# Kernel optimization log

Measured on AMD Instinct MI355X. Metric: run time of the kernel, lower is better.

The kernel has to match this reference:

```python
import jax, jax.numpy as jnp
import numpy as np
from jax import lax

B, CIN, COUT, N, H, W = 8, 64, 64, 9, 128, 128
KS, PAD = 3, 1
EPS = 1e-5
DN = ('NCHW', 'OIHW', 'NCHW')

def _conv(x, w, b, pad):
    y = lax.conv_general_dilated(x, w, (1, 1), [(pad, pad), (pad, pad)], dimension_numbers=DN)
    return y + b[None, :, None, None]

def setup_inputs() -> dict:
    key = jax.random.key(0)
    ks = jax.random.split(key, 8)
    fan = CIN * KS * KS
    s = 1.0 / np.sqrt(fan)
    return {
        'x': jax.random.normal(ks[0], (B, CIN, H, W), dtype=jnp.float32),
        'kernels_w': jax.random.uniform(ks[1], (N, COUT, CIN, KS, KS), minval=-s, maxval=s, dtype=jnp.float32),
        'kernels_b': jax.random.uniform(ks[2], (N, COUT), minval=-s, maxval=s, dtype=jnp.float32),
        'obs1_w': jax.random.uniform(ks[3], (COUT // 2, CIN, 1, 1), minval=-1/np.sqrt(CIN), maxval=1/np.sqrt(CIN), dtype=jnp.float32),
        'obs1_b': jax.random.uniform(ks[4], (COUT // 2,), minval=-1/np.sqrt(CIN), maxval=1/np.sqrt(CIN), dtype=jnp.float32),
        'obs2_w': jax.random.uniform(ks[5], (N, COUT // 2, 1, 1), minval=-1/np.sqrt(COUT // 2), maxval=1/np.sqrt(COUT // 2), dtype=jnp.float32),
        'obs2_b': jax.random.uniform(ks[6], (N,), minval=-1/np.sqrt(COUT // 2), maxval=1/np.sqrt(COUT // 2), dtype=jnp.float32),
        'gamma': jnp.ones((COUT,), dtype=jnp.float32),
        'beta': jnp.zeros((COUT,), dtype=jnp.float32),
    }

def reference(x, kernels_w, kernels_b, obs1_w, obs1_b, obs2_w, obs2_b, gamma, beta):
    b, _, h, w = x.shape
    # all N path convs as one grouped-output conv: (B, N*COUT, H, W)
    paths = _conv(x, kernels_w.reshape(N * COUT, CIN, KS, KS), kernels_b.reshape(-1), PAD)
    paths = paths.reshape(b, N, COUT, h, w)
    # observer: 1x1 conv -> tanh -> 1x1 conv, scores (B, N, H, W)
    scores = _conv(jnp.tanh(_conv(x, obs1_w, obs1_b, 0)), obs2_w, obs2_b, 0)
    # eval-mode collapse: per-pixel argmax over paths, one-hot weighted sum == gather
    idx = jnp.argmax(scores, axis=1)  # (B, H, W)
    sel = jnp.take_along_axis(paths, idx[:, None, None, :, :], axis=1)[:, 0]  # (B, COUT, H, W)
    out = jax.nn.relu(sel)
    # ModularPhaseNorm2d (assumed instance-norm-style per-channel spatial norm with affine)
    mu = jnp.mean(out, axis=(2, 3), keepdims=True)
    var = jnp.var(out, axis=(2, 3), keepdims=True)
    y = (out - mu) * lax.rsqrt(var + EPS)
    return y * gamma[None, :, None, None] + beta[None, :, None, None]
```

## Files before the change

kernel.cpp:

```cpp
#include <hip/hip_runtime.h>
#include <hip/hip_bf16.h>
#include <stdint.h>

#define B_    8
#define CIN   64
#define COUT  64
#define NPATH 9
#define H_    128
#define W_    128
#define HW    16384
#define PTOT  131072
#define NBIN  72
#define CHUNK 64
#define NBLK  256
#define MAXCHUNK 4096
#define NSCORE 1024

typedef float  f32x4   __attribute__((ext_vector_type(4)));
typedef float  f32x16  __attribute__((ext_vector_type(16)));
typedef __bf16 bf16x8  __attribute__((ext_vector_type(8)));
typedef short  short8  __attribute__((ext_vector_type(8)));
typedef unsigned short ushort4v __attribute__((ext_vector_type(4)));

__device__ __forceinline__ short f2bf(float f) {
    __bf16 b = (__bf16)f;
    return __builtin_bit_cast(short, b);
}
__device__ __forceinline__ float bf2f(unsigned short u) {
    unsigned v = ((unsigned)u) << 16;
    return __builtin_bit_cast(float, v);
}
__device__ __forceinline__ float fast_tanh(float a) {
    float e = __builtin_amdgcn_exp2f(a * 2.885390081777927f);
    return 1.0f - 2.0f / (e + 1.0f);
}

#define GC(arr, i)  ((arr)[(i) * 16])
#define SM(arr, i)  ((arr)[(i) * 16])

__global__ void k_zero(f32x4* __restrict__ dst) {
    int i = blockIdx.x * 256 + threadIdx.x;
    if (i < 5120) dst[i] = (f32x4)0.0f;
}

__global__ __launch_bounds__(256, 2) void k_pre(
                      const float* __restrict__ x,
                      const float* __restrict__ w1, const float* __restrict__ b1,
                      const float* __restrict__ w2, const float* __restrict__ b2,
                      const float* __restrict__ kw,
                      unsigned* __restrict__ gcnt, unsigned* __restrict__ lists,
                      unsigned short* __restrict__ Xb,
                      unsigned short* __restrict__ WbF) {
    int t = threadIdx.x;
    if (blockIdx.x >= NSCORE) {
        int ob = ((int)blockIdx.x - NSCORE) * 4096 + t * 16;
        #pragma unroll
        for (int j = 0; j < 16; ++j) {
            int o = ob + j;
            int jj   = o & 7;
            int lane = (o >> 3) & 63;
            int f    = (o >> 9) & 3;
            int rest = o >> 11;
            int s    = rest % 18;
            int n    = rest / 18;
            int c    = f * 16 + (lane & 15);
            int kg   = lane >> 4;
            int ci   = ((s & 1) << 5) + (kg << 3) + jj;
            int tap  = s >> 1;
            WbF[o] = (unsigned short)f2bf(kw[((n * 64 + c) * 64 + ci) * 9 + tap]);
        }
        return;
    }
    __shared__ float xt[64 * 128];
    __shared__ float ht[32 * 128];
    __shared__ float w1t[64 * 36];
    __shared__ unsigned scnt[NBIN];
    __shared__ unsigned sbase[NBIN];

    int px0 = blockIdx.x * 128;
    int b   = blockIdx.x >> 7;
    int hw0 = px0 & 16383;
    if (t < NBIN) scnt[t] = 0u;

    const float* xbp = x + (((size_t)b) << 20) + hw0;
    #pragma unroll
    for (int i = 0; i < 8; ++i) {
        int flat = i * 256 + t;
        int ch = flat >> 5, ck = flat & 31;
        f32x4 v = *(const f32x4*)(xbp + ch * HW + ck * 4);
        *(f32x4*)(&xt[ch * 128 + ck * 4]) = v;
    }
    #pragma unroll
    for (int i = 0; i < 8; ++i) {
        int flat = i * 256 + t;
        int j = flat >> 6, ch = flat & 63;
        w1t[ch * 36 + j] = w1[flat];
    }
    __syncthreads();

    int wv = t >> 6, l = t & 63;
    {
        float acc[8][2];
        #pragma unroll
        for (int jj = 0; jj < 8; ++jj) {
            float bj = b1[wv * 8 + jj];
            acc[jj][0] = bj; acc[jj][1] = bj;
        }
        #pragma unroll 8
        for (int ch = 0; ch < 64; ++ch) {
            f32x4 wa = *(const f32x4*)(&w1t[ch * 36 + wv * 8]);
            f32x4 wb = *(const f32x4*)(&w1t[ch * 36 + wv * 8 + 4]);
            float2 xx = *(const float2*)(&xt[ch * 128 + l * 2]);
            #pragma unroll
            for (int jj = 0; jj < 4; ++jj) {
                acc[jj][0]     += xx.x * wa[jj];
                acc[jj][1]     += xx.y * wa[jj];
                acc[4 + jj][0] += xx.x * wb[jj];
                acc[4 + jj][1] += xx.y * wb[jj];
            }
        }
        #pragma unroll
        for (int jj = 0; jj < 8; ++jj)
            *(float2*)(&ht[(wv * 8 + jj) * 128 + l * 2]) =
                make_float2(acc[jj][0], acc[jj][1]);
    }
    __syncthreads();

    int bin = 0; unsigned rank = 0;
    if (t < 128) {
        int px = t;
        float h[32];
        #pragma unroll
        for (int j = 0; j < 32; ++j) h[j] = fast_tanh(ht[j * 128 + px]);
        float best = -1e30f; int bi = 0;
        #pragma unroll
        for (int nn = 0; nn < 9; ++nn) {
            const f32x16 Wa = *(const f32x16*)&w2[nn * 32];
            const f32x16 Wb = *(const f32x16*)&w2[nn * 32 + 16];
            float a = b2[nn];
            #pragma unroll
            for (int i = 0; i < 16; ++i)
                a += h[i] * Wa[i] + h[16 + i] * Wb[i];
            if (a > best) { best = a; bi = nn; }
        }
        bin = bi * 8 + b;
        rank = atomicAdd(&scnt[bin], 1u);
    } else {
        int px = t - 128;
        size_t xo = ((size_t)(px0 + px)) << 6;
        #pragma unroll
        for (int v8 = 0; v8 < 8; ++v8) {
            short8 pk;
            #pragma unroll
            for (int i = 0; i < 8; ++i)
                pk[i] = f2bf(xt[(v8 * 8 + i) * 128 + px]);
            *(short8*)(Xb + xo + v8 * 8) = pk;
        }
    }
    __syncthreads();
    if (t < NBIN && scnt[t]) sbase[t] = atomicAdd(&GC(gcnt, t), scnt[t]);
    __syncthreads();
    if (t < 128) lists[bin * 16384 + sbase[bin] + rank] = (unsigned)(px0 + t);
}

__global__ void k_prefix(const unsigned* __restrict__ gcnt,
                         unsigned long long* __restrict__ chunkinfo,
                         unsigned* __restrict__ ctot) {
    __shared__ unsigned st[NBIN + 1];
    int t = threadIdx.x;
    for (int i = t; i < MAXCHUNK; i += 256) chunkinfo[i] = ~0ull;
    if (t == 0) {
        unsigned acc = 0;
        for (int bin = 0; bin < NBIN; ++bin) {
            st[bin] = acc;
            acc += (GC(gcnt, bin) + (CHUNK - 1u)) / CHUNK;
        }
        st[NBIN] = acc;
        *ctot = acc;
    }
    __syncthreads();
    if (t < NBIN) {
        unsigned c0 = st[t], cnt = GC(gcnt, t);
        unsigned nch = (cnt + (CHUNK - 1u)) / CHUNK;
        for (unsigned k = 0; k < nch; ++k)
            chunkinfo[c0 + k] = ((unsigned long long)t << 32)
                              | ((unsigned long long)cnt << 16)
                              | (unsigned long long)(k * CHUNK);
    }
}

__global__ __launch_bounds__(512, 2) void k_conv(
        const unsigned short* __restrict__ Xb, const unsigned short* __restrict__ WbF,
        const float* __restrict__ kb, const unsigned* __restrict__ lists,
        const unsigned long long* __restrict__ chunkinfo, const unsigned* __restrict__ ctot,
        unsigned short* __restrict__ Yc, float* __restrict__ sums) {
    __shared__ char blds[2][73728];
    int t = threadIdx.x;
    int wid = t >> 6, lane = t & 63, kg = lane >> 4, l15 = lane & 15;
    int f = wid & 3, gh = wid >> 2;
    int spx = t >> 3, q = t & 7;
    int sq8 = (q ^ (spx & 7)) * 8;
    int dst16 = t * 16;

    unsigned C = *ctot;
    unsigned bid = (blockIdx.x & 7) * 32 + (blockIdx.x >> 3);
    unsigned c0 = (bid * C) / NBLK, c1 = ((bid + 1) * C) / NBLK;
    if (c0 >= c1) return;

    short8 g[9];
    #define GLOAD(P) do {                                                         \
        unsigned p_ = (P);                                                        \
        int h_ = (int)((p_ >> 7) & 127u), w_ = (int)(p_ & 127u);                  \
        unsigned pb_ = p_ & ~16383u;                                              \
        _Pragma("unroll")                                                         \
        for (int k_ = 0; k_ < 9; ++k_) {                                          \
            int dh_ = k_ / 3 - 1, dw_ = k_ % 3 - 1;                               \
            int h2_ = min(max(h_ + dh_, 0), 127);                                 \
            int w2_ = min(max(w_ + dw_, 0), 127);                                 \
            g[k_] = *(const short8*)(Xb +                                         \
                ((size_t)(pb_ | (unsigned)((h2_ << 7) + w2_)) << 6) + sq8);       \
        }                                                                         \
    } while (0)

    #define DECODE(INFO, BIN, CNT, BAS) { BIN = (int)((INFO) >> 32); \
        CNT = (int)(((INFO) >> 16) & 0xFFFFu); BAS = (int)((INFO) & 0xFFFFu); }

    unsigned long long inf = chunkinfo[c0];
    int cb, cc_, cbase;
    DECODE(inf, cb, cc_, cbase);
    unsigned cps  = lists[cb * 16384 + min(cbase + spx,            cc_ - 1)];
    unsigned cpm0 = lists[cb * 16384 + min(cbase + gh * 32 + l15,      cc_ - 1)];
    unsigned cpm1 = lists[cb * 16384 + min(cbase + gh * 32 + 16 + l15, cc_ - 1)];
    GLOAD(cps);

    inf = chunkinfo[min(c0 + 1, c1 - 1)];
    int nb, nc_, nbase;
    DECODE(inf, nb, nc_, nbase);
    unsigned nps  = lists[nb * 16384 + min(nbase + spx,            nc_ - 1)];
    unsigned npm0 = lists[nb * 16384 + min(nbase + gh * 32 + l15,      nc_ - 1)];
    unsigned npm1 = lists[nb * 16384 + min(nbase + gh * 32 + 16 + l15, nc_ - 1)];
    unsigned long long inf2 = chunkinfo[min(c0 + 2, c1 - 1)];

    int n = cb >> 3, b = cb & 7;
    short8 wv[18];
    #pragma unroll
    for (int s = 0; s < 18; ++s)
        wv[s] = *(const short8*)(WbF + n * 36864 + ((s * 4 + f) * 64 + lane) * 8);
    f32x4 bias = *(const f32x4*)(kb + n * 64 + f * 16 + kg * 4);

    asm volatile("s_waitcnt vmcnt(0)" ::: "memory");
    #pragma unroll
    for (int k = 0; k < 9; ++k) *(short8*)(&blds[0][k * 8192 + dst16]) = g[k];
    asm volatile("s_waitcnt lgkmcnt(0)" ::: "memory");

    int cur = 0;
    float s1[4] = {0.f,0.f,0.f,0.f}, s2[4] = {0.f,0.f,0.f,0.f};

    for (unsigned c = c0; c < c1; ++c) {
        __builtin_amdgcn_s_barrier();
        GLOAD(nps);

        int v0 = (cbase + gh * 32 + l15)      < cc_ ? 1 : 0;
        int v1 = (cbase + gh * 32 + 16 + l15) < cc_ ? 1 : 0;
        int inb0 = 0, inb1 = 0;
        {
            int h0 = (int)((cpm0 >> 7) & 127u), w0 = (int)(cpm0 & 127u);
            int h1 = (int)((cpm1 >> 7) & 127u), w1v = (int)(cpm1 & 127u);
            #pragma unroll
            for (int tap = 0; tap < 9; ++tap) {
                int dh = tap / 3 - 1, dw = tap % 3 - 1;
                if ((unsigned)(h0 + dh) < 128u && (unsigned)(w0 + dw) < 128u) inb0 |= (1 << tap);
                if ((unsigned)(h1 + dh) < 128u && (unsigned)(w1v + dw) < 128u) inb1 |= (1 << tap);
            }
            inb0 = v0 ? inb0 : 0;
            inb1 = v1 ? inb1 : 0;
        }
        f32x4 acc0 = (f32x4)0.0f, acc1 = (f32x4)0.0f;
        const short8 zero8 = (short8)0;
        const char* bufc = blds[cur];
        int pxa = gh * 32 + l15, pxb = pxa + 16;
        #pragma unroll
        for (int s = 0; s < 18; ++s) {
            const int tap = s >> 1;
            const int pr = ((s & 1) << 2) | kg;
            bf16x8 af = __builtin_bit_cast(bf16x8, wv[s]);
            short8 ra = *(const short8*)(bufc + tap * 8192 + pxa * 128 + ((pr ^ (pxa & 7)) << 4));
            short8 rb = *(const short8*)(bufc + tap * 8192 + pxb * 128 + ((pr ^ (pxb & 7)) << 4));
            short8 sa = ((inb0 >> tap) & 1) ? ra : zero8;
            short8 sb = ((inb1 >> tap) & 1) ? rb : zero8;
            acc0 = __builtin_amdgcn_mfma_f32_16x16x32_bf16(af, __builtin_bit_cast(bf16x8, sa), acc0, 0, 0, 0);
            acc1 = __builtin_amdgcn_mfma_f32_16x16x32_bf16(af, __builtin_bit_cast(bf16x8, sb), acc1, 0, 0, 0);
        }
        {
            f32x4 o0, o1;
            #pragma unroll
            for (int r = 0; r < 4; ++r) {
                o0[r] = fmaxf(acc0[r] + bias[r], 0.0f);
                o1[r] = fmaxf(acc1[r] + bias[r], 0.0f);
            }
            if (v0) {
                ushort4v u;
                #pragma unroll
                for (int r = 0; r < 4; ++r) u[r] = (unsigned short)f2bf(o0[r]);
                *(ushort4v*)(Yc + (((size_t)cpm0) << 6) + f * 16 + kg * 4) = u;
            }
            if (v1) {
                ushort4v u;
                #pragma unroll
                for (int r = 0; r < 4; ++r) u[r] = (unsigned short)f2bf(o1[r]);
                *(ushort4v*)(Yc + (((size_t)cpm1) << 6) + f * 16 + kg * 4) = u;
            }
            #pragma unroll
            for (int r = 0; r < 4; ++r) {
                float a = v0 ? o0[r] : 0.0f, bb = v1 ? o1[r] : 0.0f;
                s1[r] += a + bb;
                s2[r] += a * a + bb * bb;
            }
        }

        int fb, fc2, fbase;
        DECODE(inf2, fb, fc2, fbase);
        unsigned fps  = lists[fb * 16384 + min(fbase + spx,            fc2 - 1)];
        unsigned fpm0 = lists[fb * 16384 + min(fbase + gh * 32 + l15,      fc2 - 1)];
        unsigned fpm1 = lists[fb * 16384 + min(fbase + gh * 32 + 16 + l15, fc2 - 1)];
        unsigned long long inf3 = chunkinfo[min(c + 3, c1 - 1)];

        asm volatile("s_waitcnt vmcnt(4)" ::: "memory");
        __builtin_amdgcn_sched_barrier(0);
        #pragma unroll
        for (int k = 0; k < 9; ++k) *(short8*)(&blds[cur ^ 1][k * 8192 + dst16]) = g[k];
        asm volatile("s_waitcnt lgkmcnt(0)" ::: "memory");
        __builtin_amdgcn_sched_barrier(0);

        if (nb != cb && c + 1 < c1) {
            float f1[4], f2[4];
            #pragma unroll
            for (int r = 0; r < 4; ++r) { f1[r] = s1[r]; f2[r] = s2[r]; s1[r] = 0.f; s2[r] = 0.f; }
            #pragma unroll
            for (int m = 1; m < 16; m <<= 1) {
                #pragma unroll
                for (int r = 0; r < 4; ++r) {
                    f1[r] += __shfl_xor(f1[r], m, 64);
                    f2[r] += __shfl_xor(f2[r], m, 64);
                }
            }
            if (l15 == 0) {
                #pragma unroll
                for (int r = 0; r < 4; ++r) {
                    int ch = f * 16 + kg * 4 + r;
                    atomicAdd(&SM(sums, b * 64 + ch),       f1[r]);
                    atomicAdd(&SM(sums, 512 + b * 64 + ch), f2[r]);
                }
            }
            n = nb >> 3; b = nb & 7;
            #pragma unroll
            for (int s = 0; s < 18; ++s)
                wv[s] = *(const short8*)(WbF + n * 36864 + ((s * 4 + f) * 64 + lane) * 8);
            bias = *(const f32x4*)(kb + n * 64 + f * 16 + kg * 4);
        }

        cb = nb; cc_ = nc_; cbase = nbase; cpm0 = npm0; cpm1 = npm1;
        nb = fb; nc_ = fc2; nbase = fbase; nps = fps; npm0 = fpm0; npm1 = fpm1;
        inf2 = inf3;
        cur ^= 1;
    }

    #pragma unroll
    for (int m = 1; m < 16; m <<= 1) {
        #pragma unroll
        for (int r = 0; r < 4; ++r) {
            s1[r] += __shfl_xor(s1[r], m, 64);
            s2[r] += __shfl_xor(s2[r], m, 64);
        }
    }
    if (l15 == 0) {
        #pragma unroll
        for (int r = 0; r < 4; ++r) {
            int ch = f * 16 + kg * 4 + r;
            atomicAdd(&SM(sums, b * 64 + ch),       s1[r]);
            atomicAdd(&SM(sums, 512 + b * 64 + ch), s2[r]);
        }
    }
    #undef GLOAD
    #undef DECODE
}

__global__ void k_final(const unsigned short* __restrict__ Yc, const float* __restrict__ sums,
                        const float* __restrict__ gamma, const float* __restrict__ beta,
                        float* __restrict__ out) {
    __shared__ float ld[128][66];
    __shared__ float smu[64], srs[64], sg[64], sb[64];
    int t = threadIdx.x;
    int b = blockIdx.y, hw0 = blockIdx.x * 128;
    if (t < 64) {
        float mu = SM(sums, b * 64 + t) * (1.0f / HW);
        float vr = SM(sums, 512 + b * 64 + t) * (1.0f / HW) - mu * mu;
        smu[t] = mu;
        srs[t] = rsqrtf(fmaxf(vr, 0.0f) + 1e-5f);
        sg[t] = gamma[t]; sb[t] = beta[t];
    }
    int i = t >> 1, half = t & 1;
    const short8* row = (const short8*)(Yc + (((size_t)(b * HW + hw0 + i)) << 6) + half * 32);
    #pragma unroll
    for (int q = 0; q < 4; ++q) {
        short8 v = row[q];
        #pragma unroll
        for (int j = 0; j < 8; ++j)
            ld[i][half * 32 + q * 8 + j] = bf2f((unsigned short)v[j]);
    }
    __syncthreads();
    #pragma unroll
    for (int rep = 0; rep < 32; ++rep) {
        int idx = rep * 256 + t;
        int c = idx >> 7, j = idx & 127;
        float v = (ld[j][c] - smu[c]) * srs[c] * sg[c] + sb[c];
        out[(((size_t)b * 64 + c) << 14) + hw0 + j] = v;
    }
}

extern "C" void kernel_launch(void* const* d_in, const int* in_sizes, int n_in,
                              void* d_out, int out_size, void* d_ws, size_t ws_size,
                              hipStream_t stream) {
    const float* x    = (const float*)d_in[0];
    const float* kw   = (const float*)d_in[1];
    const float* kb   = (const float*)d_in[2];
    const float* w1   = (const float*)d_in[3];
    const float* b1   = (const float*)d_in[4];
    const float* w2   = (const float*)d_in[5];
    const float* b2   = (const float*)d_in[6];
    const float* gam  = (const float*)d_in[7];
    const float* bet  = (const float*)d_in[8];
    float* out = (float*)d_out;

    char* ws = (char*)d_ws;
    unsigned* gcnt      = (unsigned*)(ws + 0);
    unsigned* ctot      = (unsigned*)(ws + 8192);
    float*    sums      = (float*)   (ws + 16384);
    unsigned long long* chunkinfo = (unsigned long long*)(ws + 81920);
    unsigned* lists     = (unsigned*)(ws + 131072);
    unsigned short* Yc  = (unsigned short*)(ws + 5242880);
    unsigned short* Xb  = (unsigned short*)(ws + 22020096);
    unsigned short* WbF = (unsigned short*)(ws + 38797312);

    k_zero<<<20, 256, 0, stream>>>((f32x4*)ws);
    k_pre<<<NSCORE + 81, 256, 0, stream>>>(x, w1, b1, w2, b2, kw, gcnt, lists, Xb, WbF);
    k_prefix<<<1, 256, 0, stream>>>(gcnt, chunkinfo, ctot);
    k_conv<<<NBLK, 512, 0, stream>>>(Xb, WbF, kb, lists, chunkinfo, ctot, Yc, sums);
    k_final<<<dim3(128, 8), 256, 0, stream>>>(Yc, sums, gam, bet, out);
}
```

Baseline: 83.87 us.

## Shrink conv chunks to 16 pixels with smaller blocks and more grid parallelism

```diff
diff --git a/kernel.cpp b/kernel.cpp
--- a/kernel.cpp
+++ b/kernel.cpp
@@ -11,9 +11,9 @@
 #define HW    16384
 #define PTOT  131072
 #define NBIN  72
-#define CHUNK 64
-#define NBLK  256
-#define MAXCHUNK 4096
+#define CHUNK 16
+#define NBLK  1024
+#define MAXCHUNK 9216
 #define NSCORE 1024
 
 typedef float  f32x4   __attribute__((ext_vector_type(4)));
@@ -74,6 +74,7 @@
     __shared__ float xt[64 * 128];
     __shared__ float ht[32 * 128];
     __shared__ float w1t[64 * 36];
+    __shared__ float w2s[304];
     __shared__ unsigned scnt[NBIN];
     __shared__ unsigned sbase[NBIN];
 
@@ -96,6 +97,8 @@
         int j = flat >> 6, ch = flat & 63;
         w1t[ch * 36 + j] = w1[flat];
     }
+    for (int i = t; i < 288; i += 256) w2s[i] = w2[i];
+    if (t < 9) w2s[288 + t] = b2[t];
     __syncthreads();
 
     int wv = t >> 6, l = t & 63;
@@ -135,12 +138,10 @@
         float best = -1e30f; int bi = 0;
         #pragma unroll
         for (int nn = 0; nn < 9; ++nn) {
-            const f32x16 Wa = *(const f32x16*)&w2[nn * 32];
-            const f32x16 Wb = *(const f32x16*)&w2[nn * 32 + 16];
-            float a = b2[nn];
+            float a = w2s[288 + nn];
             #pragma unroll
             for (int i = 0; i < 16; ++i)
-                a += h[i] * Wa[i] + h[16 + i] * Wb[i];
+                a += h[i] * w2s[nn * 32 + i] + h[16 + i] * w2s[nn * 32 + 16 + i];
             if (a > best) { best = a; bi = nn; }
         }
         bin = bi * 8 + b;
@@ -189,37 +190,49 @@
     }
 }
 
-__global__ __launch_bounds__(512, 2) void k_conv(
+__global__ __launch_bounds__(256, 4) void k_conv(
         const unsigned short* __restrict__ Xb, const unsigned short* __restrict__ WbF,
         const float* __restrict__ kb, const unsigned* __restrict__ lists,
         const unsigned long long* __restrict__ chunkinfo, const unsigned* __restrict__ ctot,
         unsigned short* __restrict__ Yc, float* __restrict__ sums) {
-    __shared__ char blds[2][73728];
+    __shared__ char blds[2][18432];
     int t = threadIdx.x;
     int wid = t >> 6, lane = t & 63, kg = lane >> 4, l15 = lane & 15;
-    int f = wid & 3, gh = wid >> 2;
-    int spx = t >> 3, q = t & 7;
+    int f = wid;
+    int slot = t & 127, half = t >> 7;
+    int spx = slot >> 3, q = slot & 7;
     int sq8 = (q ^ (spx & 7)) * 8;
-    int dst16 = t * 16;
+    int tap0 = half * 5;
+    int ntap = half ? 4 : 5;
 
     unsigned C = *ctot;
-    unsigned bid = (blockIdx.x & 7) * 32 + (blockIdx.x >> 3);
+    unsigned bid = (blockIdx.x & 7) * 128 + (blockIdx.x >> 3);
     unsigned c0 = (bid * C) / NBLK, c1 = ((bid + 1) * C) / NBLK;
     if (c0 >= c1) return;
 
-    short8 g[9];
+    short8 g[5];
     #define GLOAD(P) do {                                                         \
         unsigned p_ = (P);                                                        \
         int h_ = (int)((p_ >> 7) & 127u), w_ = (int)(p_ & 127u);                  \
         unsigned pb_ = p_ & ~16383u;                                              \
         _Pragma("unroll")                                                         \
-        for (int k_ = 0; k_ < 9; ++k_) {                                          \
-            int dh_ = k_ / 3 - 1, dw_ = k_ % 3 - 1;                               \
-            int h2_ = min(max(h_ + dh_, 0), 127);                                 \
-            int w2_ = min(max(w_ + dw_, 0), 127);                                 \
-            g[k_] = *(const short8*)(Xb +                                         \
-                ((size_t)(pb_ | (unsigned)((h2_ << 7) + w2_)) << 6) + sq8);       \
+        for (int k_ = 0; k_ < 5; ++k_) {                                          \
+            if (k_ < ntap) {                                                      \
+                int tap_ = tap0 + k_;                                             \
+                int dh_ = tap_ / 3 - 1, dw_ = tap_ % 3 - 1;                       \
+                int h2_ = min(max(h_ + dh_, 0), 127);                             \
+                int w2_ = min(max(w_ + dw_, 0), 127);                             \
+                g[k_] = *(const short8*)(Xb +                                     \
+                    ((size_t)(pb_ | (unsigned)((h2_ << 7) + w2_)) << 6) + sq8);   \
+            }                                                                     \
         }                                                                         \
+    } while (0)
+
+    #define DSWRITE(BUF) do {                                                     \
+        _Pragma("unroll")                                                         \
+        for (int k_ = 0; k_ < 5; ++k_)                                            \
+            if (k_ < ntap)                                                        \
+                *(short8*)(&(BUF)[(tap0 + k_) * 2048 + slot * 16]) = g[k_];       \
     } while (0)
 
     #define DECODE(INFO, BIN, CNT, BAS) { BIN = (int)((INFO) >> 32); \
@@ -228,17 +241,15 @@
     unsigned long long inf = chunkinfo[c0];
     int cb, cc_, cbase;
     DECODE(inf, cb, cc_, cbase);
-    unsigned cps  = lists[cb * 16384 + min(cbase + spx,            cc_ - 1)];
-    unsigned cpm0 = lists[cb * 16384 + min(cbase + gh * 32 + l15,      cc_ - 1)];
-    unsigned cpm1 = lists[cb * 16384 + min(cbase + gh * 32 + 16 + l15, cc_ - 1)];
+    unsigned cps = lists[cb * 16384 + min(cbase + spx, cc_ - 1)];
+    unsigned cpm = lists[cb * 16384 + min(cbase + l15, cc_ - 1)];
     GLOAD(cps);
 
     inf = chunkinfo[min(c0 + 1, c1 - 1)];
     int nb, nc_, nbase;
     DECODE(inf, nb, nc_, nbase);
-    unsigned nps  = lists[nb * 16384 + min(nbase + spx,            nc_ - 1)];
-    unsigned npm0 = lists[nb * 16384 + min(nbase + gh * 32 + l15,      nc_ - 1)];
-    unsigned npm1 = lists[nb * 16384 + min(nbase + gh * 32 + 16 + l15, nc_ - 1)];
+    unsigned nps = lists[nb * 16384 + min(nbase + spx, nc_ - 1)];
+    unsigned npm = lists[nb * 16384 + min(nbase + l15, nc_ - 1)];
     unsigned long long inf2 = chunkinfo[min(c0 + 2, c1 - 1)];
 
     int n = cb >> 3, b = cb & 7;
@@ -249,8 +260,7 @@
     f32x4 bias = *(const f32x4*)(kb + n * 64 + f * 16 + kg * 4);
 
     asm volatile("s_waitcnt vmcnt(0)" ::: "memory");
-    #pragma unroll
-    for (int k = 0; k < 9; ++k) *(short8*)(&blds[0][k * 8192 + dst16]) = g[k];
+    DSWRITE(blds[0]);
     asm volatile("s_waitcnt lgkmcnt(0)" ::: "memory");
 
     int cur = 0;
@@ -260,75 +270,57 @@
         __builtin_amdgcn_s_barrier();
         GLOAD(nps);
 
-        int v0 = (cbase + gh * 32 + l15)      < cc_ ? 1 : 0;
-        int v1 = (cbase + gh * 32 + 16 + l15) < cc_ ? 1 : 0;
-        int inb0 = 0, inb1 = 0;
+        int valid = (cbase + l15) < cc_ ? 1 : 0;
+        int inb = 0;
         {
-            int h0 = (int)((cpm0 >> 7) & 127u), w0 = (int)(cpm0 & 127u);
-            int h1 = (int)((cpm1 >> 7) & 127u), w1v = (int)(cpm1 & 127u);
+            int hh = (int)((cpm >> 7) & 127u), ww = (int)(cpm & 127u);
             #pragma unroll
             for (int tap = 0; tap < 9; ++tap) {
                 int dh = tap / 3 - 1, dw = tap % 3 - 1;
-                if ((unsigned)(h0 + dh) < 128u && (unsigned)(w0 + dw) < 128u) inb0 |= (1 << tap);
-                if ((unsigned)(h1 + dh) < 128u && (unsigned)(w1v + dw) < 128u) inb1 |= (1 << tap);
-            }
-            inb0 = v0 ? inb0 : 0;
-            inb1 = v1 ? inb1 : 0;
-        }
-        f32x4 acc0 = (f32x4)0.0f, acc1 = (f32x4)0.0f;
+                if ((unsigned)(hh + dh) < 128u && (unsigned)(ww + dw) < 128u) inb |= (1 << tap);
+            }
+            inb = valid ? inb : 0;
+        }
+        f32x4 acc = (f32x4)0.0f;
         const short8 zero8 = (short8)0;
         const char* bufc = blds[cur];
-        int pxa = gh * 32 + l15, pxb = pxa + 16;
         #pragma unroll
         for (int s = 0; s < 18; ++s) {
             const int tap = s >> 1;
             const int pr = ((s & 1) << 2) | kg;
-            bf16x8 af = __builtin_bit_cast(bf16x8, wv[s]);
-            short8 ra = *(const short8*)(bufc + tap * 8192 + pxa * 128 + ((pr ^ (pxa & 7)) << 4));
-            short8 rb = *(const short8*)(bufc + tap * 8192 + pxb * 128 + ((pr ^ (pxb & 7)) << 4));
-            short8 sa = ((inb0 >> tap) & 1) ? ra : zero8;
-            short8 sb = ((inb1 >> tap) & 1) ? rb : zero8;
-            acc0 = __builtin_amdgcn_mfma_f32_16x16x32_bf16(af, __builtin_bit_cast(bf16x8, sa), acc0, 0, 0, 0);
-            acc1 = __builtin_amdgcn_mfma_f32_16x16x32_bf16(af, __builtin_bit_cast(bf16x8, sb), acc1, 0, 0, 0);
+            short8 braw = *(const short8*)(bufc + tap * 2048 + l15 * 128 + ((pr ^ (l15 & 7)) << 4));
+            short8 sel = ((inb >> tap) & 1) ? braw : zero8;
+            acc = __builtin_amdgcn_mfma_f32_16x16x32_bf16(
+                      __builtin_bit_cast(bf16x8, wv[s]),
+                      __builtin_bit_cast(bf16x8, sel), acc, 0, 0, 0);
         }
         {
-            f32x4 o0, o1;
-            #pragma unroll
-            for (int r = 0; r < 4; ++r) {
-                o0[r] = fmaxf(acc0[r] + bias[r], 0.0f);
-                o1[r] = fmaxf(acc1[r] + bias[r], 0.0f);
-            }
-            if (v0) {
+            f32x4 o;
+            #pragma unroll
+            for (int r = 0; r < 4; ++r) o[r] = fmaxf(acc[r] + bias[r], 0.0f);
+            if (valid) {
                 ushort4v u;
                 #pragma unroll
-                for (int r = 0; r < 4; ++r) u[r] = (unsigned short)f2bf(o0[r]);
-                *(ushort4v*)(Yc + (((size_t)cpm0) << 6) + f * 16 + kg * 4) = u;
-            }
-            if (v1) {
-                ushort4v u;
-                #pragma unroll
-                for (int r = 0; r < 4; ++r) u[r] = (unsigned short)f2bf(o1[r]);
-                *(ushort4v*)(Yc + (((size_t)cpm1) << 6) + f * 16 + kg * 4) = u;
+                for (int r = 0; r < 4; ++r) u[r] = (unsigned short)f2bf(o[r]);
+                *(ushort4v*)(Yc + (((size_t)cpm) << 6) + f * 16 + kg * 4) = u;
             }
             #pragma unroll
             for (int r = 0; r < 4; ++r) {
-                float a = v0 ? o0[r] : 0.0f, bb = v1 ? o1[r] : 0.0f;
-                s1[r] += a + bb;
-                s2[r] += a * a + bb * bb;
+                float sv = valid ? o[r] : 0.0f;
+                s1[r] += sv;
+                s2[r] += sv * sv;
             }
         }
 
         int fb, fc2, fbase;
         DECODE(inf2, fb, fc2, fbase);
-        unsigned fps  = lists[fb * 16384 + min(fbase + spx,            fc2 - 1)];
-        unsigned fpm0 = lists[fb * 16384 + min(fbase + gh * 32 + l15,      fc2 - 1)];
-        unsigned fpm1 = lists[fb * 16384 + min(fbase + gh * 32 + 16 + l15, fc2 - 1)];
+        unsigned fps = lists[fb * 16384 + min(fbase + spx, fc2 - 1)];
+        unsigned fpm = lists[fb * 16384 + min(fbase + l15, fc2 - 1)];
         unsigned long long inf3 = chunkinfo[min(c + 3, c1 - 1)];
 
         asm volatile("s_waitcnt vmcnt(4)" ::: "memory");
         __builtin_amdgcn_sched_barrier(0);
-        #pragma unroll
-        for (int k = 0; k < 9; ++k) *(short8*)(&blds[cur ^ 1][k * 8192 + dst16]) = g[k];
+        DSWRITE(blds[cur ^ 1]);
         asm volatile("s_waitcnt lgkmcnt(0)" ::: "memory");
         __builtin_amdgcn_sched_barrier(0);
 
@@ -359,8 +351,8 @@
             bias = *(const f32x4*)(kb + n * 64 + f * 16 + kg * 4);
         }
 
-        cb = nb; cc_ = nc_; cbase = nbase; cpm0 = npm0; cpm1 = npm1;
-        nb = fb; nc_ = fc2; nbase = fbase; nps = fps; npm0 = fpm0; npm1 = fpm1;
+        cb = nb; cc_ = nc_; cbase = nbase; cpm = npm;
+        nb = fb; nc_ = fc2; nbase = fbase; nps = fps; npm = fpm;
         inf2 = inf3;
         cur ^= 1;
     }
@@ -382,6 +374,7 @@
         }
     }
     #undef GLOAD
+    #undef DSWRITE
     #undef DECODE
 }
 
@@ -437,7 +430,7 @@
     unsigned* ctot      = (unsigned*)(ws + 8192);
     float*    sums      = (float*)   (ws + 16384);
     unsigned long long* chunkinfo = (unsigned long long*)(ws + 81920);
-    unsigned* lists     = (unsigned*)(ws + 131072);
+    unsigned* lists     = (unsigned*)(ws + 163840);
     unsigned short* Yc  = (unsigned short*)(ws + 5242880);
     unsigned short* Xb  = (unsigned short*)(ws + 22020096);
     unsigned short* WbF = (unsigned short*)(ws + 38797312);
@@ -445,6 +438,6 @@
     k_zero<<<20, 256, 0, stream>>>((f32x4*)ws);
     k_pre<<<NSCORE + 81, 256, 0, stream>>>(x, w1, b1, w2, b2, kw, gcnt, lists, Xb, WbF);
     k_prefix<<<1, 256, 0, stream>>>(gcnt, chunkinfo, ctot);
-    k_conv<<<NBLK, 512, 0, stream>>>(Xb, WbF, kb, lists, chunkinfo, ctot, Yc, sums);
+    k_conv<<<NBLK, 256, 0, stream>>>(Xb, WbF, kb, lists, chunkinfo, ctot, Yc, sums);
     k_final<<<dim3(128, 8), 256, 0, stream>>>(Yc, sums, gam, bet, out);
 }
```

New measurement: 107.2 us. 1.28x slower.
